# Optimization experiments

Hardware: AMD Instinct MI355X
Metric: run time of the kernel (lower is better)

Reference implementation:

```python
import jax, jax.numpy as jnp
import numpy as np

B, T, Q, K = 64, 2048, 512, 512

def setup_inputs() -> dict:
    key0 = jax.random.key(0)
    k1, k2, k3 = jax.random.split(key0, 3)
    query = jax.random.normal(k1, (B, Q), dtype=jnp.float32)
    key = jax.random.normal(k2, (B, T, K), dtype=jnp.float32)
    # learned params: weights ~ U(-0.1, 0.1), bias zeros(1)
    W = jax.random.uniform(k3, (K, Q), dtype=jnp.float32) * 0.2 - 0.1
    bias = jnp.zeros((1,), dtype=jnp.float32)
    return {"query": query, "key": key, "W": W, "bias": bias}

def reference(query, key, W, bias):
    # mids = W @ query : [B, K]
    mids = jnp.einsum('kq,bq->bk', W, query)
    # scores = tanh(key . mids + bias) : [B, T]
    scores = jnp.tanh(jnp.einsum('btk,bk->bt', key, mids) + bias)
    return jax.nn.softmax(scores, axis=1)
```

## Files before the change

### kernel.cpp

```cpp
#include <hip/hip_runtime.h>
#include <math.h>

#define WAVE 64

typedef float nfloat4 __attribute__((ext_vector_type(4)));


#define LOG2E 1.44269504088896f
__device__ __forceinline__ float exp_tanh(float u) {
    float z = __builtin_amdgcn_exp2f(2.0f * LOG2E * u);
    float t = 1.0f - 2.0f * __builtin_amdgcn_rcpf(1.0f + z);
    return __builtin_amdgcn_exp2f(LOG2E * t);
}

__device__ __forceinline__ float reduce8(const float s[8]) {
    const int lane = (int)(threadIdx.x & 63);
    const bool hi32 = (lane & 32) != 0;
    float v[4];
    #pragma unroll
    for (int r = 0; r < 4; ++r) {
        float keep = hi32 ? s[r + 4] : s[r];
        float send = hi32 ? s[r] : s[r + 4];
        v[r] = keep + __shfl_xor(send, 32, WAVE);
    }
    const bool hi16 = (lane & 16) != 0;
    float w[2];
    #pragma unroll
    for (int r = 0; r < 2; ++r) {
        float keep = hi16 ? v[r + 2] : v[r];
        float send = hi16 ? v[r] : v[r + 2];
        w[r] = keep + __shfl_xor(send, 16, WAVE);
    }
    const bool hi8 = (lane & 8) != 0;
    float keep = hi8 ? w[1] : w[0];
    float send = hi8 ? w[0] : w[1];
    float x = keep + __shfl_xor(send, 8, WAVE);
    x += __shfl_xor(x, 4, WAVE);
    x += __shfl_xor(x, 2, WAVE);
    x += __shfl_xor(x, 1, WAVE);
    return x;
}

__global__ __launch_bounds__(256, 4)
void mids_kernel(const float* __restrict__ W,
                 const float* __restrict__ query,
                 float* __restrict__ mids) {
    const int gwave = (int)((blockIdx.x * blockDim.x + threadIdx.x) >> 6);
    const int lane  = threadIdx.x & 63;
    const int b  = gwave >> 6;
    const int k0 = (gwave & 63) * 8;

    const float4* qrow = (const float4*)(query + (size_t)b * 512);
    const float4 q0 = qrow[lane];
    const float4 q1 = qrow[lane + 64];

    float s[8];
    #pragma unroll
    for (int r = 0; r < 8; ++r) {
        const float4* wrow = (const float4*)(W + (size_t)(k0 + r) * 512);
        float4 a = wrow[lane];
        float4 c = wrow[lane + 64];
        s[r] = a.x*q0.x + a.y*q0.y + a.z*q0.z + a.w*q0.w
             + c.x*q1.x + c.y*q1.y + c.z*q1.z + c.w*q1.w;
    }
    float x = reduce8(s);
    if ((lane & 7) == 0)
        mids[(size_t)gwave * 8 + ((lane >> 3) & 7)] = x;
}

__global__ __launch_bounds__(256, 4)
void scores_kernel(const float* __restrict__ key,
                   const float* __restrict__ mids,
                   const float* __restrict__ bias,
                   float* __restrict__ out,
                   float* __restrict__ partial) {
    const int gwave = (int)((blockIdx.x * blockDim.x + threadIdx.x) >> 6);
    const int lane  = threadIdx.x & 63;
    const int row0  = gwave * 16;
    const int b     = row0 >> 11;

    const float4* mrow = (const float4*)(mids + (size_t)b * 512);
    const float4 m0 = mrow[lane];
    const float4 m1 = mrow[lane + 64];
    const float bv = bias[0];

    const nfloat4* kbase = (const nfloat4*)key + (size_t)row0 * 128;

    float wave_sum = 0.f;

    #pragma unroll
    for (int g = 0; g < 2; ++g) {
        const int r0 = g * 8;
        nfloat4 a[8], c[8];
        #pragma unroll
        for (int r = 0; r < 8; ++r) {
            a[r] = __builtin_nontemporal_load(&kbase[(size_t)(r0 + r) * 128 + lane]);
            c[r] = __builtin_nontemporal_load(&kbase[(size_t)(r0 + r) * 128 + lane + 64]);
        }
        float s[8];
        #pragma unroll
        for (int r = 0; r < 8; ++r) {
            s[r] = a[r].x*m0.x + a[r].y*m0.y + a[r].z*m0.z + a[r].w*m0.w
                 + c[r].x*m1.x + c[r].y*m1.y + c[r].z*m1.z + c[r].w*m1.w;
        }
        float x = reduce8(s);
        float e = exp_tanh(x + bv);
        if ((lane & 7) == 0)
            out[(size_t)row0 + r0 + ((lane >> 3) & 7)] = e;
        float y = e;
        y += __shfl_xor(y, 8, WAVE);
        y += __shfl_xor(y, 16, WAVE);
        y += __shfl_xor(y, 32, WAVE);
        wave_sum += y;
    }
    if (lane == 0)
        partial[gwave] = wave_sum;
}

__global__ __launch_bounds__(256, 4)
void normalize_kernel(float* __restrict__ out,
                      const float* __restrict__ partial) {
    const int b   = blockIdx.x;
    const int tid = threadIdx.x;

    __shared__ float red[4];

    float v = (tid < 128) ? partial[b * 128 + tid] : 0.f;
    #pragma unroll
    for (int off = 32; off > 0; off >>= 1)
        v += __shfl_xor(v, off, WAVE);
    if ((tid & 63) == 0) red[tid >> 6] = v;
    __syncthreads();
    const float inv = 1.f / (red[0] + red[1]);

    float4* row = (float4*)(out + (size_t)b * 2048);
    #pragma unroll
    for (int i = 0; i < 2; ++i) {
        float4 x = row[tid + i * 256];
        x.x *= inv; x.y *= inv; x.z *= inv; x.w *= inv;
        row[tid + i * 256] = x;
    }
}

extern "C" void kernel_launch(void* const* d_in, const int* in_sizes, int n_in,
                              void* d_out, int out_size, void* d_ws, size_t ws_size,
                              hipStream_t stream) {
    const float* query = (const float*)d_in[0];
    const float* key   = (const float*)d_in[1];
    const float* W     = (const float*)d_in[2];
    const float* bias  = (const float*)d_in[3];
    float* out  = (float*)d_out;
    float* mids = (float*)d_ws;
    float* partial = mids + 64 * 512;

    mids_kernel<<<1024, 256, 0, stream>>>(W, query, mids);

    scores_kernel<<<2048, 256, 0, stream>>>(key, mids, bias, out, partial);

    normalize_kernel<<<64, 256, 0, stream>>>(out, partial);
}
```

Baseline: 344.5 us.

## Fuse softmax normalization into scores kernel via last-block atomic counter

Removes the separate normalize kernel launch. Each scores block increments a per-batch atomic counter, and the last of the 32 blocks for a batch row reduces the partial sums and rescales that row. The counters are zeroed in mids_kernel. This saves a launch and a kernel boundary, at the cost of atomics, fences, an extra __syncthreads in every block, and a serialized tail for the last block of each batch row.

```diff
diff --git a/kernel.cpp b/kernel.cpp
--- a/kernel.cpp
+++ b/kernel.cpp
@@ -44,7 +44,10 @@
 __global__ __launch_bounds__(256, 4)
 void mids_kernel(const float* __restrict__ W,
                  const float* __restrict__ query,
-                 float* __restrict__ mids) {
+                 float* __restrict__ mids,
+                 int* __restrict__ cnt) {
+    if (blockIdx.x == 0 && threadIdx.x < 64) cnt[threadIdx.x * 32] = 0;
+
     const int gwave = (int)((blockIdx.x * blockDim.x + threadIdx.x) >> 6);
     const int lane  = threadIdx.x & 63;
     const int b  = gwave >> 6;
@@ -73,7 +76,8 @@
                    const float* __restrict__ mids,
                    const float* __restrict__ bias,
                    float* __restrict__ out,
-                   float* __restrict__ partial) {
+                   float* __restrict__ partial,
+                   int* __restrict__ cnt) {
     const int gwave = (int)((blockIdx.x * blockDim.x + threadIdx.x) >> 6);
     const int lane  = threadIdx.x & 63;
     const int row0  = gwave * 16;
@@ -115,30 +119,37 @@
     }
     if (lane == 0)
         partial[gwave] = wave_sum;
-}
 
-__global__ __launch_bounds__(256, 4)
-void normalize_kernel(float* __restrict__ out,
-                      const float* __restrict__ partial) {
-    const int b   = blockIdx.x;
-    const int tid = threadIdx.x;
+    const int bblk = (int)(blockIdx.x >> 5);
+    const int tid  = (int)threadIdx.x;
+    __shared__ int s_old;
+    __shared__ float red[2];
 
-    __shared__ float red[4];
+    __syncthreads();
+    if (tid == 0) {
+        __threadfence();
+        s_old = atomicAdd(&cnt[bblk * 32], 1);
+    }
+    __syncthreads();
+    if (s_old == 31) {
+        __threadfence();
 
-    float v = (tid < 128) ? partial[b * 128 + tid] : 0.f;
-    #pragma unroll
-    for (int off = 32; off > 0; off >>= 1)
-        v += __shfl_xor(v, off, WAVE);
-    if ((tid & 63) == 0) red[tid >> 6] = v;
-    __syncthreads();
-    const float inv = 1.f / (red[0] + red[1]);
+        float v = (tid < 128) ? partial[bblk * 128 + tid] : 0.f;
+        #pragma unroll
+        for (int off = 32; off > 0; off >>= 1)
+            v += __shfl_xor(v, off, WAVE);
+        if (tid == 0)  red[0] = v;
+        if (tid == 64) red[1] = v;
+        __syncthreads();
+        const float inv = 1.f / (red[0] + red[1]);
 
-    float4* row = (float4*)(out + (size_t)b * 2048);
-    #pragma unroll
-    for (int i = 0; i < 2; ++i) {
-        float4 x = row[tid + i * 256];
-        x.x *= inv; x.y *= inv; x.z *= inv; x.w *= inv;
-        row[tid + i * 256] = x;
+        float4* row = (float4*)(out + (size_t)bblk * 2048);
+        #pragma unroll
+        for (int i = 0; i < 2; ++i) {
+            float4 x = row[tid + i * 256];
+            x.x *= inv; x.y *= inv; x.z *= inv; x.w *= inv;
+            row[tid + i * 256] = x;
+        }
     }
 }
 
@@ -152,10 +163,9 @@
     float* out  = (float*)d_out;
     float* mids = (float*)d_ws;
     float* partial = mids + 64 * 512;
+    int*   cnt = (int*)(partial + 8192);
 
-    mids_kernel<<<1024, 256, 0, stream>>>(W, query, mids);
+    mids_kernel<<<1024, 256, 0, stream>>>(W, query, mids, cnt);
 
-    scores_kernel<<<2048, 256, 0, stream>>>(key, mids, bias, out, partial);
-
-    normalize_kernel<<<64, 256, 0, stream>>>(out, partial);
+    scores_kernel<<<2048, 256, 0, stream>>>(key, mids, bias, out, partial, cnt);
 }
```

After: 496.6 us. 1.44x slower.
